# Kernel optimization log

Hardware: AMD Instinct MI355X
Metric: run time of the kernel (lower is better)

Reference implementation:

```python
import jax, jax.numpy as jnp
import numpy as np

B = 2048
U_DIM = 128
N_USER = 500000
N_NEWS = 50000
N_WORD = 279215
TITLE_LEN = 10
W_EMB = 50
U_NB = 30   # user_neighbor
N_NB = 30   # news_neighbor
NCAPS = 8
NHID = 16
DIM = NCAPS * NHID          # 128
CNN_OUT = 128
ROUTIT = 4
CONV_CH, KH, KW = 8, 2, 20
PH, PW = 2, 1
FLAT = CONV_CH * ((TITLE_LEN - KH + 1) // PH) * (W_EMB - KW + 1)  # 8*4*31 = 992


def setup_inputs() -> dict:
    key = jax.random.key(0)
    ks = jax.random.split(key, 18)
    nrm = lambda k, s: jax.random.normal(k, s, jnp.float32) * 0.1
    return {
        "user_indices": jax.random.randint(ks[0], (B,), 0, N_USER),
        "news_indices": jax.random.randint(ks[1], (B,), 0, N_NEWS),
        "labels": (jax.random.uniform(ks[2], (B,)) > 0.5).astype(jnp.float32),
        # int neighbor / title tables (module buffers)
        "news_user": jax.random.randint(ks[3], (N_NEWS + 1, U_NB), 0, N_USER),
        "user_news": jax.random.randint(ks[4], (N_USER + 1, N_NB), 0, N_NEWS),
        "title": jax.random.randint(ks[5], (N_NEWS + 1, TITLE_LEN), 0, N_WORD),
        # float parameters
        "user_emb_matrix": nrm(ks[6], (N_USER + 1, U_DIM)),
        "word_emb_matrix": nrm(ks[7], (N_WORD + 1, W_EMB)),
        "conv_w": nrm(ks[8], (CONV_CH, 1, KH, KW)),
        "conv_b": jnp.zeros((CONV_CH,), jnp.float32),
        "dense_w": nrm(ks[9], (FLAT, CNN_OUT)),
        "dense_b": jnp.zeros((CNN_OUT,), jnp.float32),
        "user_weights": nrm(ks[10], (U_DIM, DIM)),
        "user_bias": nrm(ks[11], (DIM,)),
        "item_weights": nrm(ks[12], (CNN_OUT, DIM)),
        "item_bias": nrm(ks[13], (DIM,)),
        "last_w": nrm(ks[14], (DIM, DIM)),
        "last_b": jnp.zeros((DIM,), jnp.float32),
    }


def _convolution(news_ids, title, word_emb, conv_w, conv_b, dense_w, dense_b):
    """Title-CNN news encoder. news_ids: [B, K] int -> [B*K, CNN_OUT]."""
    bk = news_ids.shape[0] * news_ids.shape[1]
    words = title[news_ids.reshape(-1)]              # [BK, L] gather
    x = word_emb[words][:, None, :, :]               # [BK, 1, L, 50]
    y = jax.lax.conv_general_dilated(
        x, conv_w, (1, 1), 'VALID', dimension_numbers=('NCHW', 'OIHW', 'NCHW'))
    y = jax.nn.relu(y + conv_b[None, :, None, None])
    y = jax.lax.reduce_window(y, -jnp.inf, jax.lax.max,
                              (1, 1, PH, PW), (1, 1, PH, PW), 'VALID')
    return jax.nn.relu(y.reshape(bk, -1) @ dense_w + dense_b)


def _routing(x_self, z_nb):
    """Capsule neighbor routing. x_self: [B, DIM], z_nb: [B, K, DIM]."""
    l2n = lambda v: v / (jnp.linalg.norm(v, axis=-1, keepdims=True) + 1e-9)
    x = l2n(x_self.reshape(-1, NCAPS, NHID))
    z = l2n(z_nb.reshape(z_nb.shape[0], z_nb.shape[1], NCAPS, NHID))
    u = x
    for _ in range(ROUTIT):
        p = jax.nn.softmax(jnp.einsum('bkcd,bcd->bkc', z, u), axis=-1)  # over caps
        u = l2n(x + jnp.einsum('bkc,bkcd->bcd', p, z))
    return u.reshape(-1, DIM)


def reference(user_indices, news_indices, labels, news_user, user_news, title,
              user_emb_matrix, word_emb_matrix, conv_w, conv_b, dense_w, dense_b,
              user_weights, user_bias, item_weights, item_bias, last_w, last_b):
    # hop-0 (seed) vectors
    news_v0 = jax.nn.relu(
        _convolution(news_indices[:, None], title, word_emb_matrix,
                     conv_w, conv_b, dense_w, dense_b) @ item_weights + item_bias)  # [B, DIM]
    user_v0 = jax.nn.relu(user_emb_matrix[user_indices] @ user_weights + user_bias)  # [B, DIM]
    # hop-1 neighbor gathers
    news_nb = news_user[news_indices]   # [B, U_NB] user ids clicked this news
    user_nb = user_news[user_indices]   # [B, N_NB] news ids clicked by user
    news_v1 = jax.nn.relu(user_emb_matrix[news_nb] @ user_weights + user_bias)  # [B, U_NB, DIM]
    user_v1 = jax.nn.relu(
        _convolution(user_nb, title, word_emb_matrix, conv_w, conv_b,
                     dense_w, dense_b) @ item_weights + item_bias
    ).reshape(B, N_NB, DIM)
    # capsule routing aggregation
    news_emb = _routing(news_v0, news_v1)
    user_emb = _routing(user_v0, user_v1)
    # simple_dot_net scoring
    x_map = user_emb @ last_w + last_b
    y_map = news_emb @ last_w + last_b
    scores = jnp.sum(x_map * y_map, axis=-1)
    return jax.nn.sigmoid(scores)
```

## Files before the change

### kernel.cpp

```cpp
#include <hip/hip_runtime.h>
#include <hip/hip_bf16.h>
#include <math.h>

#define BSZ 2048
#define NNEWS 50000
#define U_NB 30
#define N_NB 30
#define TITLE_LEN 10
#define W_EMB 50
#define DIM 128
#define ROUTIT 4
#define FLAT2 1024
#define NJOBS (BSZ * 31)

#define CONV_BLOCKS (NNEWS / 8)
#define PREP_ELEMS (DIM * FLAT2 + 2 * DIM * DIM)
#define PREP_BLOCKS (PREP_ELEMS / 256)
#define DENSE_BLOCKS ((NNEWS + 63) / 64)
#define USER_BLOCKS (NJOBS / 32)

typedef __attribute__((ext_vector_type(8))) short bf16x8;
typedef __attribute__((ext_vector_type(4))) float f32x4;

__device__ __forceinline__ ushort bfbits(float v) {
  __hip_bfloat16 h = __float2bfloat16(v);
  ushort u;
  __builtin_memcpy(&u, &h, 2);
  return u;
}

__device__ __forceinline__ bf16x8 bfrag(const ushort* row, int s) {
  const char* p = reinterpret_cast<const char*>(row) + ((s * 2) & ~15);
  const uint4 lo = *reinterpret_cast<const uint4*>(p);
  const uint4 hi = *reinterpret_cast<const uint4*>(p + 16);
  const uint d0 = lo.x, d1 = lo.y, d2 = lo.z, d3 = lo.w;
  const uint d4 = hi.x, d5 = hi.y, d6 = hi.z, d7 = hi.w;
  const bool q2 = (s & 4) != 0;
  const uint e0 = q2 ? d2 : d0, e1 = q2 ? d3 : d1, e2 = q2 ? d4 : d2;
  const uint e3 = q2 ? d5 : d3, e4 = q2 ? d6 : d4, e5 = q2 ? d7 : d5;
  const bool q1 = (s & 2) != 0;
  const uint f0 = q1 ? e1 : e0, f1 = q1 ? e2 : e1, f2 = q1 ? e3 : e2;
  const uint f3 = q1 ? e4 : e3, f4 = q1 ? e5 : e4;
  const bool r1 = (s & 1) != 0;
  uint g[4];
  g[0] = r1 ? ((f0 >> 16) | (f1 << 16)) : f0;
  g[1] = r1 ? ((f1 >> 16) | (f2 << 16)) : f1;
  g[2] = r1 ? ((f2 >> 16) | (f3 << 16)) : f2;
  g[3] = r1 ? ((f3 >> 16) | (f4 << 16)) : f3;
  bf16x8 r;
  __builtin_memcpy(&r, g, 16);
  return r;
}

__global__ __launch_bounds__(256, 4) void k_front(
    const int* __restrict__ title, const float* __restrict__ word_emb,
    const float* __restrict__ conv_w, const float* __restrict__ conv_b,
    const float* __restrict__ dw, const float* __restrict__ iw,
    const float* __restrict__ uw, __hip_bfloat16* __restrict__ flat,
    __hip_bfloat16* __restrict__ dwt, __hip_bfloat16* __restrict__ iwt,
    __hip_bfloat16* __restrict__ uwt) {
  const int tid = threadIdx.x;

  if (blockIdx.x >= CONV_BLOCKS) {
    const int idx = ((int)blockIdx.x - CONV_BLOCKS) * 256 + tid;
    if (idx < DIM * FLAT2) {
      const int col = idx & 127, k2 = idx >> 7;
      const int i = k2 & 3, X = k2 >> 2;
      const int c = X & 7, gkq = (X >> 3) & 3, jhq = (X >> 5) & 1, h = X >> 6;
      const int j = jhq * 16 + gkq * 4 + i;
      const float v = (j < 31) ? dw[(c * 124 + h * 31 + j) * 128 + col] : 0.f;
      dwt[col * FLAT2 + k2] = __float2bfloat16(v);
    } else if (idx < DIM * FLAT2 + DIM * DIM) {
      const int j = idx - DIM * FLAT2;
      const int o = j & 127, k = j >> 7;
      iwt[o * DIM + k] = __float2bfloat16(iw[j]);
    } else if (idx < PREP_ELEMS) {
      const int j = idx - DIM * FLAT2 - DIM * DIM;
      const int o = j & 127, k = j >> 7;
      uwt[o * DIM + k] = __float2bfloat16(uw[j]);
    }
    return;
  }

  __shared__ int s_words[80];
  __shared__ __align__(16) ushort s_x[80 * 64];

  const int wv = tid >> 6, lane = tid & 63;
  const int base = blockIdx.x * 8;
  const int c = lane & 15, gk = lane >> 4;

  bf16x8 b0, b1;
#pragma unroll
  for (int i = 0; i < 8; ++i) {
    const int k = gk * 8 + i;
    float v0 = 0.f, v1 = 0.f;
    if (c < 8 && k < 20) {
      v0 = conv_w[c * 40 + k];
      v1 = conv_w[c * 40 + 20 + k];
    }
    b0[i] = (short)bfbits(v0);
    b1[i] = (short)bfbits(v1);
  }
  const float cbias = (c < 8) ? conv_b[c] : 0.f;

  if (tid < 80) s_words[tid] = title[base * TITLE_LEN + tid];
  __syncthreads();

  {
    const float2* we2 = reinterpret_cast<const float2*>(word_emb);
#pragma unroll
    for (int i = 0; i < 3; ++i) {
      const int u = tid + i * 256;
      if (u < 640) {
        const int row = u >> 3, slot = u & 7;
        ushort o[8];
#pragma unroll
        for (int p = 0; p < 4; ++p) {
          const int c2 = slot * 4 + p;
          float2 v = make_float2(0.f, 0.f);
          if (c2 < 25) v = we2[(long long)s_words[row] * 25 + c2];
          o[2 * p] = bfbits(v.x);
          o[2 * p + 1] = bfbits(v.y);
        }
        *reinterpret_cast<uint4*>(&s_x[row * 64 + slot * 8]) =
            *reinterpret_cast<const uint4*>(o);
      }
    }
  }
  __syncthreads();

  ushort* fl = reinterpret_cast<ushort*>(flat);
#pragma unroll 1
  for (int tt = 0; tt < 2; ++tt) {
    const int t = wv * 2 + tt;
    const ushort* xb = &s_x[t * 640];
    ushort* gout = &fl[(size_t)(base + t) * FLAT2];
#pragma unroll
    for (int jh = 0; jh < 2; ++jh) {
      const int s = jh * 16 + (lane & 15) + gk * 8;
      bf16x8 fprev = bfrag(xb, s);
#pragma unroll
      for (int h = 0; h < 4; ++h) {
        const bf16x8 fmid = bfrag(xb + (2 * h + 1) * 64, s);
        const bf16x8 fnext = bfrag(xb + (2 * h + 2) * 64, s);
        f32x4 d0 = (f32x4){0.f, 0.f, 0.f, 0.f};
        f32x4 d1 = (f32x4){0.f, 0.f, 0.f, 0.f};
        d0 = __builtin_amdgcn_mfma_f32_16x16x32_bf16(fprev, b0, d0, 0, 0, 0);
        d0 = __builtin_amdgcn_mfma_f32_16x16x32_bf16(fmid, b1, d0, 0, 0, 0);
        d1 = __builtin_amdgcn_mfma_f32_16x16x32_bf16(fmid, b0, d1, 0, 0, 0);
        d1 = __builtin_amdgcn_mfma_f32_16x16x32_bf16(fnext, b1, d1, 0, 0, 0);
        if (c < 8) {
          ushort w[4];
#pragma unroll
          for (int i2 = 0; i2 < 4; ++i2)
            w[i2] = bfbits(fmaxf(fmaxf(d0[i2], d1[i2]) + cbias, 0.f));
          *reinterpret_cast<uint2*>(&gout[(h * 64 + jh * 32 + gk * 8 + c) * 4]) =
              *reinterpret_cast<const uint2*>(w);
        }
        fprev = fnext;
      }
    }
  }
}

__global__ __launch_bounds__(256, 2) void k_mid(
    const __hip_bfloat16* __restrict__ flat,
    const __hip_bfloat16* __restrict__ dwt, const float* __restrict__ dense_b,
    const __hip_bfloat16* __restrict__ iwt, const float* __restrict__ item_b,
    __hip_bfloat16* __restrict__ news_cnn,
    const int* __restrict__ user_indices, const int* __restrict__ news_indices,
    const int* __restrict__ news_user, const float* __restrict__ user_emb,
    const __hip_bfloat16* __restrict__ uwt, const float* __restrict__ user_b,
    __hip_bfloat16* __restrict__ user_path) {
  __shared__ __align__(16) char lds[18432];
  const int tid = threadIdx.x;
  const int wv = tid >> 6, lane = tid & 63;
  const int fr = lane & 15, gk = lane >> 4;

  if (blockIdx.x < DENSE_BLOCKS) {
    ushort* A0 = (ushort*)lds;
    ushort* A1 = (ushort*)(lds + 9216);
    ushort* c1 = (ushort*)lds;

    const int lrow0 = min((int)blockIdx.x * 64, NNEWS - 64);
    const ushort* fl = (const ushort*)flat;
    const ushort* dwp = (const ushort*)dwt;

    uint4 pA[2];
#define LD_A(KS)                                                              \
  {                                                                           \
    _Pragma("unroll") for (int q = 0; q < 2; ++q) {                           \
      const int uu = tid + q * 256;                                           \
      pA[q] = *reinterpret_cast<const uint4*>(                                \
          &fl[(size_t)(lrow0 + (uu >> 3)) * FLAT2 + (KS) * 64 + (uu & 7) * 8]); \
    }                                                                         \
  }
#define ST_A(BUF)                                                             \
  {                                                                           \
    _Pragma("unroll") for (int q = 0; q < 2; ++q) {                           \
      const int uu = tid + q * 256;                                           \
      *reinterpret_cast<uint4*>(&(BUF)[(uu >> 3) * 72 + (uu & 7) * 8]) = pA[q]; \
    }                                                                         \
  }
#define LD_B(DST, KS)                                                         \
  {                                                                           \
    _Pragma("unroll") for (int nn = 0; nn < 2; ++nn)                          \
        _Pragma("unroll") for (int qq = 0; qq < 2; ++qq) {                    \
      (DST)[nn * 2 + qq] = *reinterpret_cast<const bf16x8*>(                  \
          &dwp[(wv * 32 + nn * 16 + fr) * FLAT2 + (KS) * 64 + qq * 32 +       \
               gk * 8]);                                                      \
    }                                                                         \
  }

    LD_A(0);
    ST_A(A0);
    LD_A(1);
    bf16x8 bA[4];
    LD_B(bA, 0);
    __syncthreads();

    f32x4 acc[4][2];
#pragma unroll
    for (int m = 0; m < 4; ++m)
#pragma unroll
      for (int n2 = 0; n2 < 2; ++n2) acc[m][n2] = (f32x4){0.f, 0.f, 0.f, 0.f};

    for (int ks = 0; ks < 16; ++ks) {
      const ushort* cA = (ks & 1) ? A1 : A0;
      bf16x8 bN[4];
      if (ks < 15) {
        LD_B(bN, ks + 1);
      } else {
#pragma unroll
        for (int z = 0; z < 4; ++z) bN[z] = bA[z];
      }
      bf16x8 af[2][4];
#pragma unroll
      for (int kk = 0; kk < 2; ++kk)
#pragma unroll
        for (int m = 0; m < 4; ++m)
          af[kk][m] = *reinterpret_cast<const bf16x8*>(
              &cA[(m * 16 + fr) * 72 + kk * 32 + gk * 8]);
#pragma unroll
      for (int kk = 0; kk < 2; ++kk)
#pragma unroll
        for (int m = 0; m < 4; ++m)
#pragma unroll
          for (int n2 = 0; n2 < 2; ++n2)
            acc[m][n2] = __builtin_amdgcn_mfma_f32_16x16x32_bf16(
                af[kk][m], bA[n2 * 2 + kk], acc[m][n2], 0, 0, 0);
      if (ks < 15) {
        if (ks & 1) {
          ST_A(A0);
        } else {
          ST_A(A1);
        }
      }
      if (ks < 14) LD_A(ks + 2);
      __syncthreads();
#pragma unroll
      for (int z = 0; z < 4; ++z) bA[z] = bN[z];
    }
#undef LD_A
#undef ST_A
#undef LD_B

#pragma unroll
    for (int n2 = 0; n2 < 2; ++n2) {
      const int col = wv * 32 + n2 * 16 + fr;
      const float bb = dense_b[col];
#pragma unroll
      for (int m = 0; m < 4; ++m)
#pragma unroll
        for (int r = 0; r < 4; ++r)
          c1[(m * 16 + gk * 4 + r) * 136 + col] =
              bfbits(fmaxf(acc[m][n2][r] + bb, 0.f));
    }
    __syncthreads();

    const ushort* iwp = (const ushort*)iwt;
    f32x4 a2[4][2];
#pragma unroll
    for (int m = 0; m < 4; ++m)
#pragma unroll
      for (int n2 = 0; n2 < 2; ++n2) a2[m][n2] = (f32x4){0.f, 0.f, 0.f, 0.f};
#pragma unroll
    for (int kk = 0; kk < 4; ++kk) {
      bf16x8 af[4], bfr[2];
#pragma unroll
      for (int m = 0; m < 4; ++m)
        af[m] = *reinterpret_cast<const bf16x8*>(
            &c1[(m * 16 + fr) * 136 + kk * 32 + gk * 8]);
#pragma unroll
      for (int n2 = 0; n2 < 2; ++n2)
        bfr[n2] = *reinterpret_cast<const bf16x8*>(
            &iwp[(wv * 32 + n2 * 16 + fr) * DIM + kk * 32 + gk * 8]);
#pragma unroll
      for (int m = 0; m < 4; ++m)
#pragma unroll
        for (int n2 = 0; n2 < 2; ++n2)
          a2[m][n2] = __builtin_amdgcn_mfma_f32_16x16x32_bf16(
              af[m], bfr[n2], a2[m][n2], 0, 0, 0);
    }

#pragma unroll
    for (int n2 = 0; n2 < 2; ++n2) {
      const int col = wv * 32 + n2 * 16 + fr;
      const float bb = item_b[col];
#pragma unroll
      for (int m = 0; m < 4; ++m)
#pragma unroll
        for (int r = 0; r < 4; ++r) {
          const int row = m * 16 + gk * 4 + r;
          news_cnn[(size_t)(lrow0 + row) * DIM + col] =
              __float2bfloat16(fmaxf(a2[m][n2][r] + bb, 0.f));
        }
    }
    return;
  }

  __hip_bfloat16* s_e = (__hip_bfloat16*)lds;
  int* s_uid = (int*)(lds + 8704);
  const int base = ((int)blockIdx.x - DENSE_BLOCKS) * 32;

  if (tid < 32) {
    const int r = base + tid;
    int uid;
    if (r < BSZ) {
      uid = user_indices[r];
    } else {
      const int j = r - BSZ;
      const int b = j / U_NB, k = j - b * U_NB;
      uid = news_user[(long long)news_indices[b] * U_NB + k];
    }
    s_uid[tid] = uid;
  }
  __syncthreads();
#pragma unroll
  for (int i = 0; i < 4; ++i) {
    const int u = tid + i * 256;
    const int row = u >> 5, d4 = u & 31;
    const float4 v = *reinterpret_cast<const float4*>(
        &user_emb[(long long)s_uid[row] * DIM + d4 * 4]);
    __hip_bfloat16* p = &s_e[row * 136 + d4 * 4];
    p[0] = __float2bfloat16(v.x);
    p[1] = __float2bfloat16(v.y);
    p[2] = __float2bfloat16(v.z);
    p[3] = __float2bfloat16(v.w);
  }
  __syncthreads();

  const ushort* uwp = (const ushort*)uwt;
  f32x4 acc[2][2];
#pragma unroll
  for (int m = 0; m < 2; ++m)
#pragma unroll
    for (int n = 0; n < 2; ++n) acc[m][n] = (f32x4){0.f, 0.f, 0.f, 0.f};

#pragma unroll
  for (int ks = 0; ks < 4; ++ks) {
    bf16x8 af[2], bfr[2];
#pragma unroll
    for (int m = 0; m < 2; ++m)
      af[m] = *reinterpret_cast<const bf16x8*>(
          &s_e[(m * 16 + fr) * 136 + ks * 32 + gk * 8]);
#pragma unroll
    for (int n = 0; n < 2; ++n)
      bfr[n] = *reinterpret_cast<const bf16x8*>(
          &uwp[(wv * 32 + n * 16 + fr) * DIM + ks * 32 + gk * 8]);
#pragma unroll
    for (int m = 0; m < 2; ++m)
#pragma unroll
      for (int n = 0; n < 2; ++n)
        acc[m][n] = __builtin_amdgcn_mfma_f32_16x16x32_bf16(af[m], bfr[n],
                                                            acc[m][n], 0, 0, 0);
  }

#pragma unroll
  for (int n = 0; n < 2; ++n) {
    const int col = wv * 32 + n * 16 + fr;
    const float bb = user_b[col];
#pragma unroll
    for (int m = 0; m < 2; ++m)
#pragma unroll
      for (int r = 0; r < 4; ++r) {
        const int row = m * 16 + gk * 4 + r;
        user_path[(size_t)(base + row) * DIM + col] =
            __float2bfloat16(fmaxf(acc[m][n][r] + bb, 0.f));
      }
  }
}

__device__ __forceinline__ float gsum16(float v) {
  v += __shfl_xor(v, 1, 16);
  v += __shfl_xor(v, 2, 16);
  v += __shfl_xor(v, 4, 16);
  v += __shfl_xor(v, 8, 16);
  return v;
}

__global__ __launch_bounds__(512) void k_back(
    const __hip_bfloat16* __restrict__ news_cnn,
    const __hip_bfloat16* __restrict__ user_path,
    const int* __restrict__ user_indices, const int* __restrict__ news_indices,
    const int* __restrict__ user_news, const float* __restrict__ last_w,
    const float* __restrict__ last_b, float* __restrict__ out) {
  __shared__ int s_nid[32];
  __shared__ __align__(16) float zf2[2][30][132];
  __shared__ __align__(16) float xn2[2][128];
  __shared__ __align__(16) float uu2[2][128];
  __shared__ __align__(16) float pp2[2][30][8];
  __shared__ float s_r[2];

  const int b = blockIdx.x, tid = threadIdx.x;
  const int hs = tid >> 8;
  const int t = tid & 255;
  const bool is_news = (hs == 0);
  float(*zf)[132] = zf2[hs];
  float* xn = xn2[hs];
  float* uu = uu2[hs];
  float(*pp)[8] = pp2[hs];

  if (!is_news && t < 30)
    s_nid[t] = user_news[(long long)user_indices[b] * N_NB + t];
  __syncthreads();

  const __hip_bfloat16* zsrc = is_news ? user_path : news_cnn;
  if (t < 240) {
    const int k = t >> 3, q = t & 7;
    const int zid = is_news ? (BSZ + b * 30 + k) : s_nid[k];
    const ushort* src =
        reinterpret_cast<const ushort*>(zsrc + (long long)zid * DIM);
    ushort h16[16];
    *reinterpret_cast<uint4*>(&h16[0]) =
        *reinterpret_cast<const uint4*>(&src[q * 16]);
    *reinterpret_cast<uint4*>(&h16[8]) =
        *reinterpret_cast<const uint4*>(&src[q * 16 + 8]);
    float f[16];
#pragma unroll
    for (int i = 0; i < 16; ++i) {
      const uint bits = ((uint)h16[i]) << 16;
      __builtin_memcpy(&f[i], &bits, 4);
    }
#pragma unroll
    for (int v4 = 0; v4 < 4; ++v4)
      *reinterpret_cast<f32x4*>(&zf[k][q * 16 + v4 * 4]) =
          *reinterpret_cast<f32x4*>(&f[v4 * 4]);
  }
  if (t < 128) {
    const __hip_bfloat16* xrow =
        is_news ? news_cnn + (long long)news_indices[b] * DIM
                : user_path + (long long)b * DIM;
    float xv = __bfloat162float(xrow[t]);
    xv = xv / (sqrtf(gsum16(xv * xv)) + 1e-9f);
    xn[t] = xv;
    uu[t] = xv;
  }
  __syncthreads();

  const int kk = t >> 3, cc = t & 7;
  float z16[16];
  if (t < 240) {
    float ss = 0.f;
#pragma unroll
    for (int d = 0; d < 16; ++d) {
      z16[d] = zf[kk][cc * 16 + d];
      ss += z16[d] * z16[d];
    }
    const float inv = 1.f / (sqrtf(ss) + 1e-9f);
#pragma unroll
    for (int d = 0; d < 16; ++d) {
      z16[d] *= inv;
      zf[kk][cc * 16 + d] = z16[d];
    }
  }
  __syncthreads();

  for (int it = 0; it < ROUTIT; ++it) {
    if (t < 240) {
      float dot = 0.f;
#pragma unroll
      for (int d = 0; d < 16; ++d) dot += z16[d] * uu[cc * 16 + d];
      pp[kk][cc] = dot;
    }
    __syncthreads();
    if (t < 30) {
      float m = -1e30f, e[8], s = 0.f;
#pragma unroll
      for (int c2 = 0; c2 < 8; ++c2) m = fmaxf(m, pp[t][c2]);
#pragma unroll
      for (int c2 = 0; c2 < 8; ++c2) {
        e[c2] = expf(pp[t][c2] - m);
        s += e[c2];
      }
      const float invs = 1.f / s;
#pragma unroll
      for (int c2 = 0; c2 < 8; ++c2) pp[t][c2] = e[c2] * invs;
    }
    __syncthreads();
    if (t < 128) {
      const int c2 = t >> 4;
      float agg = xn[t];
#pragma unroll
      for (int k = 0; k < 30; ++k) agg += pp[k][c2] * zf[k][t];
      uu[t] = agg / (sqrtf(gsum16(agg * agg)) + 1e-9f);
    }
    __syncthreads();
  }

  if (tid < 128) {
    float xm = last_b[tid], ym = xm;
    for (int k = 0; k < DIM; k += 4) {
#pragma unroll
      for (int i = 0; i < 4; ++i) {
        const float w = last_w[(k + i) * DIM + tid];
        xm += uu2[1][k + i] * w;
        ym += uu2[0][k + i] * w;
      }
    }
    float prod = xm * ym;
#pragma unroll
    for (int off = 1; off < 64; off <<= 1) prod += __shfl_xor(prod, off, 64);
    if ((tid & 63) == 0) s_r[tid >> 6] = prod;
  }
  __syncthreads();
  if (tid == 0) out[b] = 1.f / (1.f + expf(-(s_r[0] + s_r[1])));
}

extern "C" void kernel_launch(void* const* d_in, const int* in_sizes, int n_in,
                              void* d_out, int out_size, void* d_ws,
                              size_t ws_size, hipStream_t stream) {
  (void)in_sizes; (void)n_in; (void)out_size; (void)ws_size;
  const int* user_indices = (const int*)d_in[0];
  const int* news_indices = (const int*)d_in[1];
  const int* news_user = (const int*)d_in[3];
  const int* user_news = (const int*)d_in[4];
  const int* title = (const int*)d_in[5];
  const float* user_emb_matrix = (const float*)d_in[6];
  const float* word_emb_matrix = (const float*)d_in[7];
  const float* conv_w = (const float*)d_in[8];
  const float* conv_b = (const float*)d_in[9];
  const float* dense_w = (const float*)d_in[10];
  const float* dense_b = (const float*)d_in[11];
  const float* user_weights = (const float*)d_in[12];
  const float* user_bias = (const float*)d_in[13];
  const float* item_weights = (const float*)d_in[14];
  const float* item_bias = (const float*)d_in[15];
  const float* last_w = (const float*)d_in[16];
  const float* last_b = (const float*)d_in[17];

  char* ws = (char*)d_ws;
  __hip_bfloat16* flat = (__hip_bfloat16*)ws;
  ws += (size_t)NNEWS * FLAT2 * 2;
  __hip_bfloat16* news_cnn = (__hip_bfloat16*)ws;
  ws += (size_t)NNEWS * DIM * 2;
  __hip_bfloat16* user_path = (__hip_bfloat16*)ws;
  ws += (size_t)NJOBS * DIM * 2;
  __hip_bfloat16* dwt = (__hip_bfloat16*)ws;
  ws += (size_t)DIM * FLAT2 * 2;
  __hip_bfloat16* iwt = (__hip_bfloat16*)ws;
  ws += (size_t)DIM * DIM * 2;
  __hip_bfloat16* uwt = (__hip_bfloat16*)ws;
  float* out = (float*)d_out;

  k_front<<<CONV_BLOCKS + PREP_BLOCKS, 256, 0, stream>>>(
      title, word_emb_matrix, conv_w, conv_b, dense_w, item_weights,
      user_weights, flat, dwt, iwt, uwt);
  k_mid<<<DENSE_BLOCKS + USER_BLOCKS, 256, 0, stream>>>(
      flat, dwt, dense_b, iwt, item_bias, news_cnn, user_indices, news_indices,
      news_user, user_emb_matrix, uwt, user_bias, user_path);
  k_back<<<BSZ, 512, 0, stream>>>(news_cnn, user_path, user_indices,
                                  news_indices, user_news, last_w, last_b,
                                  out);
}
```

Before: 188.1 us.

## Fuse user-embedding projection into routing kernel and use shuffle softmax

Moves the user-path GEMM (user embedding gather and projection for each batch row's 31 users) out of the middle kernel and into the per-batch routing kernel. The 31 projected rows go straight into shared memory, so the user_path workspace round-trip through global memory goes away. The routing softmax is rewritten to use 8-lane shuffles instead of a separate sync phase, which removes one barrier per iteration. The trade-off is that the back kernel now does its own GEMM with uwt loads per block, and one row of the 32-row tile is computed redundantly.

```diff
diff --git a/kernel.cpp b/kernel.cpp
--- a/kernel.cpp
+++ b/kernel.cpp
@@ -11,13 +11,11 @@
 #define DIM 128
 #define ROUTIT 4
 #define FLAT2 1024
-#define NJOBS (BSZ * 31)
 
 #define CONV_BLOCKS (NNEWS / 8)
 #define PREP_ELEMS (DIM * FLAT2 + 2 * DIM * DIM)
 #define PREP_BLOCKS (PREP_ELEMS / 256)
 #define DENSE_BLOCKS ((NNEWS + 63) / 64)
-#define USER_BLOCKS (NJOBS / 32)
 
 typedef __attribute__((ext_vector_type(8))) short bf16x8;
 typedef __attribute__((ext_vector_type(4))) float f32x4;
@@ -163,30 +161,24 @@
   }
 }
 
-__global__ __launch_bounds__(256, 2) void k_mid(
+__global__ __launch_bounds__(256, 2) void k_dense(
     const __hip_bfloat16* __restrict__ flat,
     const __hip_bfloat16* __restrict__ dwt, const float* __restrict__ dense_b,
     const __hip_bfloat16* __restrict__ iwt, const float* __restrict__ item_b,
-    __hip_bfloat16* __restrict__ news_cnn,
-    const int* __restrict__ user_indices, const int* __restrict__ news_indices,
-    const int* __restrict__ news_user, const float* __restrict__ user_emb,
-    const __hip_bfloat16* __restrict__ uwt, const float* __restrict__ user_b,
-    __hip_bfloat16* __restrict__ user_path) {
+    __hip_bfloat16* __restrict__ news_cnn) {
   __shared__ __align__(16) char lds[18432];
+  ushort* A0 = (ushort*)lds;
+  ushort* A1 = (ushort*)(lds + 9216);
+  ushort* c1 = (ushort*)lds;
+
   const int tid = threadIdx.x;
   const int wv = tid >> 6, lane = tid & 63;
   const int fr = lane & 15, gk = lane >> 4;
-
-  if (blockIdx.x < DENSE_BLOCKS) {
-    ushort* A0 = (ushort*)lds;
-    ushort* A1 = (ushort*)(lds + 9216);
-    ushort* c1 = (ushort*)lds;
-
-    const int lrow0 = min((int)blockIdx.x * 64, NNEWS - 64);
-    const ushort* fl = (const ushort*)flat;
-    const ushort* dwp = (const ushort*)dwt;
-
-    uint4 pA[2];
+  const int lrow0 = min((int)blockIdx.x * 64, NNEWS - 64);
+  const ushort* fl = (const ushort*)flat;
+  const ushort* dwp = (const ushort*)dwt;
+
+  uint4 pA[2];
 #define LD_A(KS)                                                              \
   {                                                                           \
     _Pragma("unroll") for (int q = 0; q < 2; ++q) {                           \
@@ -212,181 +204,108 @@
     }                                                                         \
   }
 
-    LD_A(0);
-    ST_A(A0);
-    LD_A(1);
-    bf16x8 bA[4];
-    LD_B(bA, 0);
+  LD_A(0);
+  ST_A(A0);
+  LD_A(1);
+  bf16x8 bA[4];
+  LD_B(bA, 0);
+  __syncthreads();
+
+  f32x4 acc[4][2];
+#pragma unroll
+  for (int m = 0; m < 4; ++m)
+#pragma unroll
+    for (int n2 = 0; n2 < 2; ++n2) acc[m][n2] = (f32x4){0.f, 0.f, 0.f, 0.f};
+
+  for (int ks = 0; ks < 16; ++ks) {
+    const ushort* cA = (ks & 1) ? A1 : A0;
+    bf16x8 bN[4];
+    if (ks < 15) {
+      LD_B(bN, ks + 1);
+    } else {
+#pragma unroll
+      for (int z = 0; z < 4; ++z) bN[z] = bA[z];
+    }
+    bf16x8 af[2][4];
+#pragma unroll
+    for (int kk = 0; kk < 2; ++kk)
+#pragma unroll
+      for (int m = 0; m < 4; ++m)
+        af[kk][m] = *reinterpret_cast<const bf16x8*>(
+            &cA[(m * 16 + fr) * 72 + kk * 32 + gk * 8]);
+#pragma unroll
+    for (int kk = 0; kk < 2; ++kk)
+#pragma unroll
+      for (int m = 0; m < 4; ++m)
+#pragma unroll
+        for (int n2 = 0; n2 < 2; ++n2)
+          acc[m][n2] = __builtin_amdgcn_mfma_f32_16x16x32_bf16(
+              af[kk][m], bA[n2 * 2 + kk], acc[m][n2], 0, 0, 0);
+    if (ks < 15) {
+      if (ks & 1) {
+        ST_A(A0);
+      } else {
+        ST_A(A1);
+      }
+    }
+    if (ks < 14) LD_A(ks + 2);
     __syncthreads();
-
-    f32x4 acc[4][2];
-#pragma unroll
-    for (int m = 0; m < 4; ++m)
-#pragma unroll
-      for (int n2 = 0; n2 < 2; ++n2) acc[m][n2] = (f32x4){0.f, 0.f, 0.f, 0.f};
-
-    for (int ks = 0; ks < 16; ++ks) {
-      const ushort* cA = (ks & 1) ? A1 : A0;
-      bf16x8 bN[4];
-      if (ks < 15) {
-        LD_B(bN, ks + 1);
-      } else {
-#pragma unroll
-        for (int z = 0; z < 4; ++z) bN[z] = bA[z];
-      }
-      bf16x8 af[2][4];
-#pragma unroll
-      for (int kk = 0; kk < 2; ++kk)
-#pragma unroll
-        for (int m = 0; m < 4; ++m)
-          af[kk][m] = *reinterpret_cast<const bf16x8*>(
-              &cA[(m * 16 + fr) * 72 + kk * 32 + gk * 8]);
-#pragma unroll
-      for (int kk = 0; kk < 2; ++kk)
-#pragma unroll
-        for (int m = 0; m < 4; ++m)
-#pragma unroll
-          for (int n2 = 0; n2 < 2; ++n2)
-            acc[m][n2] = __builtin_amdgcn_mfma_f32_16x16x32_bf16(
-                af[kk][m], bA[n2 * 2 + kk], acc[m][n2], 0, 0, 0);
-      if (ks < 15) {
-        if (ks & 1) {
-          ST_A(A0);
-        } else {
-          ST_A(A1);
-        }
-      }
-      if (ks < 14) LD_A(ks + 2);
-      __syncthreads();
-#pragma unroll
-      for (int z = 0; z < 4; ++z) bA[z] = bN[z];
-    }
+#pragma unroll
+    for (int z = 0; z < 4; ++z) bA[z] = bN[z];
+  }
 #undef LD_A
 #undef ST_A
 #undef LD_B
 
 #pragma unroll
-    for (int n2 = 0; n2 < 2; ++n2) {
-      const int col = wv * 32 + n2 * 16 + fr;
-      const float bb = dense_b[col];
-#pragma unroll
-      for (int m = 0; m < 4; ++m)
-#pragma unroll
-        for (int r = 0; r < 4; ++r)
-          c1[(m * 16 + gk * 4 + r) * 136 + col] =
-              bfbits(fmaxf(acc[m][n2][r] + bb, 0.f));
-    }
-    __syncthreads();
-
-    const ushort* iwp = (const ushort*)iwt;
-    f32x4 a2[4][2];
+  for (int n2 = 0; n2 < 2; ++n2) {
+    const int col = wv * 32 + n2 * 16 + fr;
+    const float bb = dense_b[col];
 #pragma unroll
     for (int m = 0; m < 4; ++m)
 #pragma unroll
-      for (int n2 = 0; n2 < 2; ++n2) a2[m][n2] = (f32x4){0.f, 0.f, 0.f, 0.f};
-#pragma unroll
-    for (int kk = 0; kk < 4; ++kk) {
-      bf16x8 af[4], bfr[2];
-#pragma unroll
-      for (int m = 0; m < 4; ++m)
-        af[m] = *reinterpret_cast<const bf16x8*>(
-            &c1[(m * 16 + fr) * 136 + kk * 32 + gk * 8]);
+      for (int r = 0; r < 4; ++r)
+        c1[(m * 16 + gk * 4 + r) * 136 + col] =
+            bfbits(fmaxf(acc[m][n2][r] + bb, 0.f));
+  }
+  __syncthreads();
+
+  const ushort* iwp = (const ushort*)iwt;
+  f32x4 a2[4][2];
+#pragma unroll
+  for (int m = 0; m < 4; ++m)
+#pragma unroll
+    for (int n2 = 0; n2 < 2; ++n2) a2[m][n2] = (f32x4){0.f, 0.f, 0.f, 0.f};
+#pragma unroll
+  for (int kk = 0; kk < 4; ++kk) {
+    bf16x8 af[4], bfr[2];
+#pragma unroll
+    for (int m = 0; m < 4; ++m)
+      af[m] = *reinterpret_cast<const bf16x8*>(
+          &c1[(m * 16 + fr) * 136 + kk * 32 + gk * 8]);
+#pragma unroll
+    for (int n2 = 0; n2 < 2; ++n2)
+      bfr[n2] = *reinterpret_cast<const bf16x8*>(
+          &iwp[(wv * 32 + n2 * 16 + fr) * DIM + kk * 32 + gk * 8]);
+#pragma unroll
+    for (int m = 0; m < 4; ++m)
 #pragma unroll
       for (int n2 = 0; n2 < 2; ++n2)
-        bfr[n2] = *reinterpret_cast<const bf16x8*>(
-            &iwp[(wv * 32 + n2 * 16 + fr) * DIM + kk * 32 + gk * 8]);
-#pragma unroll
-      for (int m = 0; m < 4; ++m)
-#pragma unroll
-        for (int n2 = 0; n2 < 2; ++n2)
-          a2[m][n2] = __builtin_amdgcn_mfma_f32_16x16x32_bf16(
-              af[m], bfr[n2], a2[m][n2], 0, 0, 0);
-    }
-
-#pragma unroll
-    for (int n2 = 0; n2 < 2; ++n2) {
-      const int col = wv * 32 + n2 * 16 + fr;
-      const float bb = item_b[col];
-#pragma unroll
-      for (int m = 0; m < 4; ++m)
-#pragma unroll
-        for (int r = 0; r < 4; ++r) {
-          const int row = m * 16 + gk * 4 + r;
-          news_cnn[(size_t)(lrow0 + row) * DIM + col] =
-              __float2bfloat16(fmaxf(a2[m][n2][r] + bb, 0.f));
-        }
-    }
-    return;
-  }
-
-  __hip_bfloat16* s_e = (__hip_bfloat16*)lds;
-  int* s_uid = (int*)(lds + 8704);
-  const int base = ((int)blockIdx.x - DENSE_BLOCKS) * 32;
-
-  if (tid < 32) {
-    const int r = base + tid;
-    int uid;
-    if (r < BSZ) {
-      uid = user_indices[r];
-    } else {
-      const int j = r - BSZ;
-      const int b = j / U_NB, k = j - b * U_NB;
-      uid = news_user[(long long)news_indices[b] * U_NB + k];
-    }
-    s_uid[tid] = uid;
-  }
-  __syncthreads();
-#pragma unroll
-  for (int i = 0; i < 4; ++i) {
-    const int u = tid + i * 256;
-    const int row = u >> 5, d4 = u & 31;
-    const float4 v = *reinterpret_cast<const float4*>(
-        &user_emb[(long long)s_uid[row] * DIM + d4 * 4]);
-    __hip_bfloat16* p = &s_e[row * 136 + d4 * 4];
-    p[0] = __float2bfloat16(v.x);
-    p[1] = __float2bfloat16(v.y);
-    p[2] = __float2bfloat16(v.z);
-    p[3] = __float2bfloat16(v.w);
-  }
-  __syncthreads();
-
-  const ushort* uwp = (const ushort*)uwt;
-  f32x4 acc[2][2];
-#pragma unroll
-  for (int m = 0; m < 2; ++m)
-#pragma unroll
-    for (int n = 0; n < 2; ++n) acc[m][n] = (f32x4){0.f, 0.f, 0.f, 0.f};
-
-#pragma unroll
-  for (int ks = 0; ks < 4; ++ks) {
-    bf16x8 af[2], bfr[2];
-#pragma unroll
-    for (int m = 0; m < 2; ++m)
-      af[m] = *reinterpret_cast<const bf16x8*>(
-          &s_e[(m * 16 + fr) * 136 + ks * 32 + gk * 8]);
-#pragma unroll
-    for (int n = 0; n < 2; ++n)
-      bfr[n] = *reinterpret_cast<const bf16x8*>(
-          &uwp[(wv * 32 + n * 16 + fr) * DIM + ks * 32 + gk * 8]);
-#pragma unroll
-    for (int m = 0; m < 2; ++m)
-#pragma unroll
-      for (int n = 0; n < 2; ++n)
-        acc[m][n] = __builtin_amdgcn_mfma_f32_16x16x32_bf16(af[m], bfr[n],
-                                                            acc[m][n], 0, 0, 0);
-  }
-
-#pragma unroll
-  for (int n = 0; n < 2; ++n) {
-    const int col = wv * 32 + n * 16 + fr;
-    const float bb = user_b[col];
-#pragma unroll
-    for (int m = 0; m < 2; ++m)
+        a2[m][n2] = __builtin_amdgcn_mfma_f32_16x16x32_bf16(
+            af[m], bfr[n2], a2[m][n2], 0, 0, 0);
+  }
+
+#pragma unroll
+  for (int n2 = 0; n2 < 2; ++n2) {
+    const int col = wv * 32 + n2 * 16 + fr;
+    const float bb = item_b[col];
+#pragma unroll
+    for (int m = 0; m < 4; ++m)
 #pragma unroll
       for (int r = 0; r < 4; ++r) {
         const int row = m * 16 + gk * 4 + r;
-        user_path[(size_t)(base + row) * DIM + col] =
-            __float2bfloat16(fmaxf(acc[m][n][r] + bb, 0.f));
+        news_cnn[(size_t)(lrow0 + row) * DIM + col] =
+            __float2bfloat16(fmaxf(a2[m][n2][r] + bb, 0.f));
       }
   }
 }
@@ -401,11 +320,14 @@
 
 __global__ __launch_bounds__(512) void k_back(
     const __hip_bfloat16* __restrict__ news_cnn,
-    const __hip_bfloat16* __restrict__ user_path,
-    const int* __restrict__ user_indices, const int* __restrict__ news_indices,
+    const float* __restrict__ user_emb, const __hip_bfloat16* __restrict__ uwt,
+    const float* __restrict__ user_b, const int* __restrict__ user_indices,
+    const int* __restrict__ news_indices, const int* __restrict__ news_user,
     const int* __restrict__ user_news, const float* __restrict__ last_w,
     const float* __restrict__ last_b, float* __restrict__ out) {
+  __shared__ int s_uid[32];
   __shared__ int s_nid[32];
+  __shared__ __align__(16) __hip_bfloat16 s_e[32][136];
   __shared__ __align__(16) float zf2[2][30][132];
   __shared__ __align__(16) float xn2[2][128];
   __shared__ __align__(16) float uu2[2][128];
@@ -413,89 +335,175 @@
   __shared__ float s_r[2];
 
   const int b = blockIdx.x, tid = threadIdx.x;
+
+  if (tid < 32) {
+    int uid;
+    if (tid == 0 || tid == 31)
+      uid = user_indices[b];
+    else
+      uid = news_user[(long long)news_indices[b] * U_NB + (tid - 1)];
+    s_uid[tid] = uid;
+  }
+  if (tid >= 64 && tid < 94)
+    s_nid[tid - 64] = user_news[(long long)user_indices[b] * N_NB + (tid - 64)];
+  __syncthreads();
+
   const int hs = tid >> 8;
   const int t = tid & 255;
-  const bool is_news = (hs == 0);
   float(*zf)[132] = zf2[hs];
   float* xn = xn2[hs];
   float* uu = uu2[hs];
   float(*pp)[8] = pp2[hs];
 
-  if (!is_news && t < 30)
-    s_nid[t] = user_news[(long long)user_indices[b] * N_NB + t];
-  __syncthreads();
-
-  const __hip_bfloat16* zsrc = is_news ? user_path : news_cnn;
-  if (t < 240) {
-    const int k = t >> 3, q = t & 7;
-    const int zid = is_news ? (BSZ + b * 30 + k) : s_nid[k];
-    const ushort* src =
-        reinterpret_cast<const ushort*>(zsrc + (long long)zid * DIM);
-    ushort h16[16];
-    *reinterpret_cast<uint4*>(&h16[0]) =
-        *reinterpret_cast<const uint4*>(&src[q * 16]);
-    *reinterpret_cast<uint4*>(&h16[8]) =
-        *reinterpret_cast<const uint4*>(&src[q * 16 + 8]);
-    float f[16];
-#pragma unroll
-    for (int i = 0; i < 16; ++i) {
-      const uint bits = ((uint)h16[i]) << 16;
-      __builtin_memcpy(&f[i], &bits, 4);
-    }
-#pragma unroll
-    for (int v4 = 0; v4 < 4; ++v4)
-      *reinterpret_cast<f32x4*>(&zf[k][q * 16 + v4 * 4]) =
-          *reinterpret_cast<f32x4*>(&f[v4 * 4]);
+  if (tid < 256) {
+#pragma unroll
+    for (int i = 0; i < 4; ++i) {
+      const int u = tid + i * 256;
+      const int row = u >> 5, d4 = u & 31;
+      const float4 v = *reinterpret_cast<const float4*>(
+          &user_emb[(long long)s_uid[row] * DIM + d4 * 4]);
+      __hip_bfloat16* p = &s_e[row][d4 * 4];
+      p[0] = __float2bfloat16(v.x);
+      p[1] = __float2bfloat16(v.y);
+      p[2] = __float2bfloat16(v.z);
+      p[3] = __float2bfloat16(v.w);
+    }
+  } else {
+    if (t < 240) {
+      const int k = t >> 3, q = t & 7;
+      const ushort* src =
+          reinterpret_cast<const ushort*>(news_cnn + (long long)s_nid[k] * DIM);
+      ushort h16[16];
+      *reinterpret_cast<uint4*>(&h16[0]) =
+          *reinterpret_cast<const uint4*>(&src[q * 16]);
+      *reinterpret_cast<uint4*>(&h16[8]) =
+          *reinterpret_cast<const uint4*>(&src[q * 16 + 8]);
+      float f[16];
+#pragma unroll
+      for (int i = 0; i < 16; ++i) {
+        const uint bits = ((uint)h16[i]) << 16;
+        __builtin_memcpy(&f[i], &bits, 4);
+      }
+#pragma unroll
+      for (int v4 = 0; v4 < 4; ++v4)
+        *reinterpret_cast<f32x4*>(&zf2[1][k][q * 16 + v4 * 4]) =
+            *reinterpret_cast<f32x4*>(&f[v4 * 4]);
+    } else {
+      const int j = t - 240;
+      const ushort* src = reinterpret_cast<const ushort*>(
+          news_cnn + (long long)news_indices[b] * DIM);
+      ushort h8[8];
+      *reinterpret_cast<uint4*>(h8) =
+          *reinterpret_cast<const uint4*>(&src[j * 8]);
+#pragma unroll
+      for (int i = 0; i < 8; ++i) {
+        const uint bits = ((uint)h8[i]) << 16;
+        float fv;
+        __builtin_memcpy(&fv, &bits, 4);
+        xn2[0][j * 8 + i] = fv;
+      }
+    }
+  }
+  __syncthreads();
+
+  float z16[16];
+  const int kk = t >> 3, cc = t & 7;
+  if (tid < 256) {
+    const int wv = tid >> 6, lane = tid & 63;
+    const int fr = lane & 15, gk = lane >> 4;
+    const ushort* uwp = (const ushort*)uwt;
+    f32x4 acc[2][2];
+#pragma unroll
+    for (int m = 0; m < 2; ++m)
+#pragma unroll
+      for (int n = 0; n < 2; ++n) acc[m][n] = (f32x4){0.f, 0.f, 0.f, 0.f};
+#pragma unroll
+    for (int ks = 0; ks < 4; ++ks) {
+      bf16x8 af[2], bfr[2];
+#pragma unroll
+      for (int m = 0; m < 2; ++m)
+        af[m] = *reinterpret_cast<const bf16x8*>(
+            &s_e[m * 16 + fr][ks * 32 + gk * 8]);
+#pragma unroll
+      for (int n = 0; n < 2; ++n)
+        bfr[n] = *reinterpret_cast<const bf16x8*>(
+            &uwp[(wv * 32 + n * 16 + fr) * DIM + ks * 32 + gk * 8]);
+#pragma unroll
+      for (int m = 0; m < 2; ++m)
+#pragma unroll
+        for (int n = 0; n < 2; ++n)
+          acc[m][n] = __builtin_amdgcn_mfma_f32_16x16x32_bf16(
+              af[m], bfr[n], acc[m][n], 0, 0, 0);
+    }
+#pragma unroll
+    for (int n = 0; n < 2; ++n) {
+      const int col = wv * 32 + n * 16 + fr;
+      const float bb = user_b[col];
+#pragma unroll
+      for (int m = 0; m < 2; ++m)
+#pragma unroll
+        for (int r = 0; r < 4; ++r) {
+          const int row = m * 16 + gk * 4 + r;
+          const float val = fmaxf(acc[m][n][r] + bb, 0.f);
+          if (row == 0)
+            xn2[1][col] = val;
+          else if (row < 31)
+            zf2[0][row - 1][col] = val;
+        }
+    }
+  } else if (t < 240) {
+    float ss = 0.f;
+#pragma unroll
+    for (int d = 0; d < 16; ++d) {
+      z16[d] = zf2[1][kk][cc * 16 + d];
+      ss += z16[d] * z16[d];
+    }
+    const float inv = 1.f / (sqrtf(ss) + 1e-9f);
+#pragma unroll
+    for (int d = 0; d < 16; ++d) {
+      z16[d] *= inv;
+      zf2[1][kk][cc * 16 + d] = z16[d];
+    }
+  }
+  __syncthreads();
+
+  if (hs == 0 && t < 240) {
+    float ss = 0.f;
+#pragma unroll
+    for (int d = 0; d < 16; ++d) {
+      z16[d] = zf2[0][kk][cc * 16 + d];
+      ss += z16[d] * z16[d];
+    }
+    const float inv = 1.f / (sqrtf(ss) + 1e-9f);
+#pragma unroll
+    for (int d = 0; d < 16; ++d) {
+      z16[d] *= inv;
+      zf2[0][kk][cc * 16 + d] = z16[d];
+    }
   }
   if (t < 128) {
-    const __hip_bfloat16* xrow =
-        is_news ? news_cnn + (long long)news_indices[b] * DIM
-                : user_path + (long long)b * DIM;
-    float xv = __bfloat162float(xrow[t]);
+    float xv = xn[t];
     xv = xv / (sqrtf(gsum16(xv * xv)) + 1e-9f);
     xn[t] = xv;
     uu[t] = xv;
   }
   __syncthreads();
 
-  const int kk = t >> 3, cc = t & 7;
-  float z16[16];
-  if (t < 240) {
-    float ss = 0.f;
-#pragma unroll
-    for (int d = 0; d < 16; ++d) {
-      z16[d] = zf[kk][cc * 16 + d];
-      ss += z16[d] * z16[d];
-    }
-    const float inv = 1.f / (sqrtf(ss) + 1e-9f);
-#pragma unroll
-    for (int d = 0; d < 16; ++d) {
-      z16[d] *= inv;
-      zf[kk][cc * 16 + d] = z16[d];
-    }
-  }
-  __syncthreads();
-
   for (int it = 0; it < ROUTIT; ++it) {
     if (t < 240) {
       float dot = 0.f;
 #pragma unroll
       for (int d = 0; d < 16; ++d) dot += z16[d] * uu[cc * 16 + d];
-      pp[kk][cc] = dot;
-    }
-    __syncthreads();
-    if (t < 30) {
-      float m = -1e30f, e[8], s = 0.f;
-#pragma unroll
-      for (int c2 = 0; c2 < 8; ++c2) m = fmaxf(m, pp[t][c2]);
-#pragma unroll
-      for (int c2 = 0; c2 < 8; ++c2) {
-        e[c2] = expf(pp[t][c2] - m);
-        s += e[c2];
-      }
-      const float invs = 1.f / s;
-#pragma unroll
-      for (int c2 = 0; c2 < 8; ++c2) pp[t][c2] = e[c2] * invs;
+      float m8 = dot;
+      m8 = fmaxf(m8, __shfl_xor(m8, 1, 8));
+      m8 = fmaxf(m8, __shfl_xor(m8, 2, 8));
+      m8 = fmaxf(m8, __shfl_xor(m8, 4, 8));
+      float e = expf(dot - m8);
+      float s8 = e;
+      s8 += __shfl_xor(s8, 1, 8);
+      s8 += __shfl_xor(s8, 2, 8);
+      s8 += __shfl_xor(s8, 4, 8);
+      pp[kk][cc] = e / s8;
     }
     __syncthreads();
     if (t < 128) {
@@ -554,8 +562,6 @@
   ws += (size_t)NNEWS * FLAT2 * 2;
   __hip_bfloat16* news_cnn = (__hip_bfloat16*)ws;
   ws += (size_t)NNEWS * DIM * 2;
-  __hip_bfloat16* user_path = (__hip_bfloat16*)ws;
-  ws += (size_t)NJOBS * DIM * 2;
   __hip_bfloat16* dwt = (__hip_bfloat16*)ws;
   ws += (size_t)DIM * FLAT2 * 2;
   __hip_bfloat16* iwt = (__hip_bfloat16*)ws;
@@ -566,10 +572,9 @@
   k_front<<<CONV_BLOCKS + PREP_BLOCKS, 256, 0, stream>>>(
       title, word_emb_matrix, conv_w, conv_b, dense_w, item_weights,
       user_weights, flat, dwt, iwt, uwt);
-  k_mid<<<DENSE_BLOCKS + USER_BLOCKS, 256, 0, stream>>>(
-      flat, dwt, dense_b, iwt, item_bias, news_cnn, user_indices, news_indices,
-      news_user, user_emb_matrix, uwt, user_bias, user_path);
-  k_back<<<BSZ, 512, 0, stream>>>(news_cnn, user_path, user_indices,
-                                  news_indices, user_news, last_w, last_b,
-                                  out);
-}
+  k_dense<<<DENSE_BLOCKS, 256, 0, stream>>>(flat, dwt, dense_b, iwt, item_bias,
+                                            news_cnn);
+  k_back<<<BSZ, 512, 0, stream>>>(news_cnn, user_emb_matrix, uwt, user_bias,
+                                  user_indices, news_indices, news_user,
+                                  user_news, last_w, last_b, out);
+}
```

After: 188.0 us. No clear change (-0.0%).
